# Kernel tuning notes

Measured on AMD Instinct MI355X. Metric: run time of the kernel, lower is better.

## Reference

```python
import jax, jax.numpy as jnp
import numpy as np

N_NODES = 100000
N_REL = 500
N_EDGES = 600000
DIM = 128


def setup_inputs() -> dict:
    key = jax.random.key(0)
    ks = jax.random.split(key, 10)
    ent = jax.random.normal(ks[0], (N_NODES, DIM), dtype=jnp.float32)
    rel = jax.random.normal(ks[1], (N_REL, DIM), dtype=jnp.float32)
    edge_index = jax.random.randint(ks[2], (2, N_EDGES), 0, N_NODES, dtype=jnp.int64)
    edge_type = jax.random.randint(ks[3], (N_EDGES,), 0, N_REL, dtype=jnp.int64)
    s = 1.0 / np.sqrt(DIM)
    W_self = jax.random.uniform(ks[4], (DIM, DIM), jnp.float32, -s, s)
    b_self = jax.random.uniform(ks[5], (DIM,), jnp.float32, -s, s)
    W_nei = jax.random.uniform(ks[6], (DIM, DIM), jnp.float32, -s, s)
    b_nei = jax.random.uniform(ks[7], (DIM,), jnp.float32, -s, s)
    W_rel = jax.random.uniform(ks[8], (DIM, DIM), jnp.float32, -s, s)
    b_rel = jax.random.uniform(ks[9], (DIM,), jnp.float32, -s, s)
    return {
        "ent": ent, "rel": rel, "edge_index": edge_index, "edge_type": edge_type,
        "W_self": W_self, "b_self": b_self,
        "W_nei": W_nei, "b_nei": b_nei,
        "W_rel": W_rel, "b_rel": b_rel,
    }


def reference(ent, rel, edge_index, edge_type, W_self, b_self, W_nei, b_nei, W_rel, b_rel):
    src, dst = edge_index[0], edge_index[1]
    # gather -> sigmoid-gate -> scatter-add
    msg = ent[src] * jax.nn.sigmoid(rel[edge_type])          # [E, dim]
    agg = jax.ops.segment_sum(msg, dst, num_segments=ent.shape[0])  # [N, dim]
    out_ent = jax.nn.relu(ent @ W_self.T + b_self + agg @ W_nei.T + b_nei)
    out_rel = rel @ W_rel.T + b_rel
    return (out_ent, out_rel)
```

## Files before the change

### kernel.cpp

```cpp
#include <hip/hip_runtime.h>
#include <hip/hip_bf16.h>
#include <math.h>

#define DIM 128

typedef __bf16 bf8 __attribute__((ext_vector_type(8)));
typedef float f4 __attribute__((ext_vector_type(4)));

struct __align__(8) bf16x4 { __hip_bfloat162 a, b; };

__global__ __launch_bounds__(256) void prep_kernel(
    const float* __restrict__ rel,
    const float* __restrict__ Ws,
    const float* __restrict__ Wn,
    const float* __restrict__ Wr,
    __hip_bfloat16* __restrict__ sigb,
    __hip_bfloat16* __restrict__ Wcat,
    float* __restrict__ Wt_rel,
    int* __restrict__ offs,
    int nSig, int sigBlocks, int N) {
    int b = blockIdx.x;
    if (b < sigBlocks) {
        int i = b * 256 + threadIdx.x;
        if (i < nSig) {
            float x = rel[i];
            sigb[i] = __float2bfloat16(1.0f / (1.0f + expf(-x)));
        }
    } else if (b < sigBlocks + 32) {
        int idx = (b - sigBlocks) * 256 + threadIdx.x;
        int j  = idx >> 6;
        int k0 = (idx & 63) * 4;
        const float* src = (k0 < DIM) ? &Ws[j * DIM + k0] : &Wn[j * DIM + (k0 - DIM)];
        float4 v = *(const float4*)src;
        bf16x4 o;
        o.a.x = __float2bfloat16(v.x);
        o.a.y = __float2bfloat16(v.y);
        o.b.x = __float2bfloat16(v.z);
        o.b.y = __float2bfloat16(v.w);
        *(bf16x4*)&Wcat[(size_t)j * 256 + k0] = o;
    } else if (b < sigBlocks + 32 + 64) {
        int id = (b - sigBlocks - 32) * 256 + threadIdx.x;
        int k = id >> 7;
        int j = id & 127;
        Wt_rel[id] = Wr[j * DIM + k];
    } else {
        int i = (b - sigBlocks - 32 - 64) * 256 + threadIdx.x;
        if (i <= N) offs[i] = 0;
    }
}

__global__ __launch_bounds__(256) void conv_hist_kernel(
    const float* __restrict__ ent,
    __hip_bfloat16* __restrict__ xcat,
    const int* __restrict__ edge_index,
    int* __restrict__ counts,
    int N, int E, int convBlocks) {
    if ((int)blockIdx.x < convBlocks) {
        long long tid = (long long)blockIdx.x * 256 + threadIdx.x;
        int row = (int)(tid >> 5);
        int q   = (int)(tid & 31);
        if (row >= N) return;
        float4 v = *(const float4*)&ent[(size_t)row * DIM + q * 4];
        bf16x4 o;
        o.a.x = __float2bfloat16(v.x);
        o.a.y = __float2bfloat16(v.y);
        o.b.x = __float2bfloat16(v.z);
        o.b.y = __float2bfloat16(v.w);
        *(bf16x4*)&xcat[(size_t)row * 256 + q * 4] = o;
    } else {
        int e = (blockIdx.x - convBlocks) * 256 + threadIdx.x;
        if (e < E) atomicAdd(&counts[edge_index[E + e]], 1);
    }
}

#define SCAN_TPB 256
#define SCAN_IPT 4
#define SCAN_IPB 1024

__global__ void scan_pass1(int* __restrict__ data,
                           int* __restrict__ blockSums, int N) {
    __shared__ int ts[SCAN_TPB];
    int t = threadIdx.x;
    int base = blockIdx.x * SCAN_IPB + t * SCAN_IPT;
    int v[SCAN_IPT];
    int s = 0;
    #pragma unroll
    for (int i = 0; i < SCAN_IPT; ++i) {
        int idx = base + i;
        v[i] = (idx < N) ? data[idx] : 0;
        s += v[i];
    }
    ts[t] = s;
    __syncthreads();
    for (int off = 1; off < SCAN_TPB; off <<= 1) {
        int x = (t >= off) ? ts[t - off] : 0;
        __syncthreads();
        ts[t] += x;
        __syncthreads();
    }
    int excl = ts[t] - s;
    #pragma unroll
    for (int i = 0; i < SCAN_IPT; ++i) {
        int idx = base + i;
        if (idx < N) data[idx] = excl;
        excl += v[i];
    }
    if (t == SCAN_TPB - 1) blockSums[blockIdx.x] = ts[t];
}

__global__ void scan_pass2(int* __restrict__ blockSums, int nb) {
    __shared__ int s[128];
    int t = threadIdx.x;
    int v = (t < nb) ? blockSums[t] : 0;
    s[t] = v;
    __syncthreads();
    for (int off = 1; off < 128; off <<= 1) {
        int x = (t >= off) ? s[t - off] : 0;
        __syncthreads();
        s[t] += x;
        __syncthreads();
    }
    if (t < nb) blockSums[t] = s[t] - v;
}

__global__ void scan_pass3(int* __restrict__ offs, const int* __restrict__ blockSums,
                           int* __restrict__ cursor, int N, int E) {
    int i = blockIdx.x * blockDim.x + threadIdx.x;
    if (i < N) {
        int o = offs[i] + blockSums[i >> 10];
        offs[i] = o;
        cursor[i] = o;
    }
    if (i == 0) offs[N] = E;
}

__global__ void scatter_ids_kernel(const int* __restrict__ edge_index,
                                   const int* __restrict__ edge_type,
                                   int* __restrict__ cursor,
                                   unsigned* __restrict__ spack, int E) {
    int e = blockIdx.x * blockDim.x + threadIdx.x;
    if (e >= E) return;
    int dst = edge_index[E + e];
    int p = atomicAdd(&cursor[dst], 1);
    spack[p] = (unsigned)edge_index[e] | ((unsigned)edge_type[e] << 17);
}

__global__ __launch_bounds__(256) void aggregate_kernel(
    const __hip_bfloat16* __restrict__ xcat,
    const __hip_bfloat16* __restrict__ sigb,
    const int* __restrict__ offs,
    const unsigned* __restrict__ spack,
    __hip_bfloat16* __restrict__ xcat_w, int N) {
    int wid  = (int)((blockIdx.x * (long long)blockDim.x + threadIdx.x) >> 6);
    int lane = threadIdx.x & 63;
    if (wid >= N) return;
    int beg = offs[wid], end = offs[wid + 1];
    float ax0 = 0.f, ay0 = 0.f, ax1 = 0.f, ay1 = 0.f;
    for (int e = beg; e < end; e += 4) {
        int r = end - e;
        unsigned p0 = spack[e];
        unsigned p1 = spack[r > 1 ? e + 1 : e];
        unsigned p2 = spack[r > 2 ? e + 2 : e];
        unsigned p3 = spack[r > 3 ? e + 3 : e];
        __hip_bfloat162 v0 = *(const __hip_bfloat162*)&xcat[(size_t)(p0 & 0x1FFFFu) * 256 + lane * 2];
        __hip_bfloat162 v1 = *(const __hip_bfloat162*)&xcat[(size_t)(p1 & 0x1FFFFu) * 256 + lane * 2];
        __hip_bfloat162 v2 = *(const __hip_bfloat162*)&xcat[(size_t)(p2 & 0x1FFFFu) * 256 + lane * 2];
        __hip_bfloat162 v3 = *(const __hip_bfloat162*)&xcat[(size_t)(p3 & 0x1FFFFu) * 256 + lane * 2];
        __hip_bfloat162 g0 = *(const __hip_bfloat162*)&sigb[(size_t)(p0 >> 17) * DIM + lane * 2];
        __hip_bfloat162 g1 = *(const __hip_bfloat162*)&sigb[(size_t)(p1 >> 17) * DIM + lane * 2];
        __hip_bfloat162 g2 = *(const __hip_bfloat162*)&sigb[(size_t)(p2 >> 17) * DIM + lane * 2];
        __hip_bfloat162 g3 = *(const __hip_bfloat162*)&sigb[(size_t)(p3 >> 17) * DIM + lane * 2];
        float m1 = (r > 1) ? 1.f : 0.f;
        float m2 = (r > 2) ? 1.f : 0.f;
        float m3 = (r > 3) ? 1.f : 0.f;
        ax0 += __bfloat162float(v0.x) * __bfloat162float(g0.x);
        ay0 += __bfloat162float(v0.y) * __bfloat162float(g0.y);
        ax1 += m1 * (__bfloat162float(v1.x) * __bfloat162float(g1.x));
        ay1 += m1 * (__bfloat162float(v1.y) * __bfloat162float(g1.y));
        ax0 += m2 * (__bfloat162float(v2.x) * __bfloat162float(g2.x));
        ay0 += m2 * (__bfloat162float(v2.y) * __bfloat162float(g2.y));
        ax1 += m3 * (__bfloat162float(v3.x) * __bfloat162float(g3.x));
        ay1 += m3 * (__bfloat162float(v3.y) * __bfloat162float(g3.y));
    }
    __hip_bfloat162 o;
    o.x = __float2bfloat16(ax0 + ax1);
    o.y = __float2bfloat16(ay0 + ay1);
    *(__hip_bfloat162*)&xcat_w[(size_t)wid * 256 + 128 + lane * 2] = o;
}

__global__ __launch_bounds__(128) void relout_kernel(
    const float* __restrict__ rel,
    const float* __restrict__ Wt_rel,
    const float* __restrict__ b_rel,
    float* __restrict__ out_rel) {
    __shared__ float rrow[DIM];
    int b = blockIdx.x;
    int t = threadIdx.x;
    rrow[t] = rel[(size_t)b * DIM + t];
    __syncthreads();
    float acc = b_rel[t];
    #pragma unroll 8
    for (int k = 0; k < DIM; ++k) {
        acc += rrow[k] * Wt_rel[k * DIM + t];
    }
    out_rel[(size_t)b * DIM + t] = acc;
}

__global__ __launch_bounds__(256) void gemm_mfma_kernel(
    const __hip_bfloat16* xcat,
    const __hip_bfloat16* __restrict__ Wcat,
    const float* __restrict__ b_self,
    const float* __restrict__ b_nei,
    float* out, int N) {
    __shared__ __hip_bfloat16 Bs[128][264];

    int t    = threadIdx.x;
    int wave = t >> 6;
    int lane = t & 63;
    int quad = lane >> 4;
    int r16  = lane & 15;

    {
        int r = t >> 1, h = t & 1;
        const float4* src = (const float4*)&Wcat[(size_t)r * 256 + h * 128];
        #pragma unroll
        for (int i = 0; i < 16; ++i) {
            *(float4*)&Bs[r][h * 128 + i * 8] = src[i];
        }
    }
    __syncthreads();

    int row0 = blockIdx.x * 128 + wave * 32;

    bf8 x[2][8];
    #pragma unroll
    for (int mt = 0; mt < 2; ++mt) {
        int m = row0 + mt * 16 + r16;
        if (m > N - 1) m = N - 1;
        const __hip_bfloat16* xp = &xcat[(size_t)m * 256 + quad * 8];
        #pragma unroll
        for (int ks = 0; ks < 8; ++ks) {
            x[mt][ks] = *(const bf8*)(xp + ks * 32);
        }
    }

    f4 acc[2][8];
    #pragma unroll
    for (int mt = 0; mt < 2; ++mt)
        #pragma unroll
        for (int jt = 0; jt < 8; ++jt)
            acc[mt][jt] = (f4){0.f, 0.f, 0.f, 0.f};

    #pragma unroll
    for (int ks = 0; ks < 8; ++ks) {
        #pragma unroll
        for (int jt = 0; jt < 8; ++jt) {
            bf8 w = *(const bf8*)&Bs[jt * 16 + r16][ks * 32 + quad * 8];
            acc[0][jt] = __builtin_amdgcn_mfma_f32_16x16x32_bf16(w, x[0][ks], acc[0][jt], 0, 0, 0);
            acc[1][jt] = __builtin_amdgcn_mfma_f32_16x16x32_bf16(w, x[1][ks], acc[1][jt], 0, 0, 0);
        }
    }

    f4 bias4[8];
    #pragma unroll
    for (int jt = 0; jt < 8; ++jt) {
        const float4 bs = *(const float4*)&b_self[jt * 16 + quad * 4];
        const float4 bn = *(const float4*)&b_nei[jt * 16 + quad * 4];
        bias4[jt] = (f4){bs.x + bn.x, bs.y + bn.y, bs.z + bn.z, bs.w + bn.w};
    }

    #pragma unroll
    for (int mt = 0; mt < 2; ++mt) {
        int m = row0 + mt * 16 + r16;
        if (m < N) {
            #pragma unroll
            for (int jt = 0; jt < 8; ++jt) {
                f4 v = acc[mt][jt] + bias4[jt];
                float4 o;
                o.x = fmaxf(v[0], 0.f);
                o.y = fmaxf(v[1], 0.f);
                o.z = fmaxf(v[2], 0.f);
                o.w = fmaxf(v[3], 0.f);
                *(float4*)&out[(size_t)m * DIM + jt * 16 + quad * 4] = o;
            }
        }
    }
}

extern "C" void kernel_launch(void* const* d_in, const int* in_sizes, int n_in,
                              void* d_out, int out_size, void* d_ws, size_t ws_size,
                              hipStream_t stream) {
    const float* ent        = (const float*)d_in[0];
    const float* rel        = (const float*)d_in[1];
    const int*   edge_index = (const int*)d_in[2];
    const int*   edge_type  = (const int*)d_in[3];
    const float* W_self     = (const float*)d_in[4];
    const float* b_self     = (const float*)d_in[5];
    const float* W_nei      = (const float*)d_in[6];
    const float* b_nei      = (const float*)d_in[7];
    const float* W_rel      = (const float*)d_in[8];
    const float* b_rel      = (const float*)d_in[9];

    const int N = in_sizes[0] / DIM;
    const int R = in_sizes[1] / DIM;
    const int E = in_sizes[3];

    float* out     = (float*)d_out;
    float* out_rel = out + (size_t)N * DIM;
    __hip_bfloat16* xcat = (__hip_bfloat16*)d_out;

    __hip_bfloat16* sigb = (__hip_bfloat16*)d_ws;
    float* Wt_rel  = (float*)(sigb + (size_t)R * DIM);
    __hip_bfloat16* Wcat = (__hip_bfloat16*)(Wt_rel + DIM * DIM);
    int*   offs    = (int*)(Wcat + 128 * 256);
    int*   cursor  = offs + (N + 8);
    int*   bsums   = cursor + (N + 8);
    unsigned* spack = (unsigned*)(bsums + 128);

    const int nSig = R * DIM;
    const int sigBlocks = (nSig + 255) / 256;
    const int zeroBlocks = (N + 1 + 255) / 256;
    const int scanBlocks = (N + SCAN_IPB - 1) / SCAN_IPB;

    prep_kernel<<<sigBlocks + 32 + 64 + zeroBlocks, 256, 0, stream>>>(
        rel, W_self, W_nei, W_rel, sigb, Wcat, Wt_rel, offs, nSig, sigBlocks, N);

    {
        int convBlocks = (int)(((long long)N * 32 + 255) / 256);
        int histBlocks = (E + 255) / 256;
        conv_hist_kernel<<<convBlocks + histBlocks, 256, 0, stream>>>(
            ent, xcat, edge_index, offs, N, E, convBlocks);
    }

    scan_pass1<<<scanBlocks, SCAN_TPB, 0, stream>>>(offs, bsums, N);
    scan_pass2<<<1, 128, 0, stream>>>(bsums, scanBlocks);
    scan_pass3<<<(N + 255) / 256, 256, 0, stream>>>(offs, bsums, cursor, N, E);

    scatter_ids_kernel<<<(E + 255) / 256, 256, 0, stream>>>(
        edge_index, edge_type, cursor, spack, E);

    {
        long long threads = (long long)N * 64;
        aggregate_kernel<<<(int)((threads + 255) / 256), 256, 0, stream>>>(
            xcat, sigb, offs, spack, xcat, N);
    }

    relout_kernel<<<R, DIM, 0, stream>>>(rel, Wt_rel, b_rel, out_rel);

    {
        int blocks = (N + 127) / 128;
        gemm_mfma_kernel<<<blocks, 256, 0, stream>>>(xcat, Wcat, b_self, b_nei, out, N);
    }
}
```

Measured before the change: 252.6 us.

## Record edge ranks in histogram, merge scan passes, fuse relout into aggregation

```diff
diff --git a/kernel.cpp b/kernel.cpp
--- a/kernel.cpp
+++ b/kernel.cpp
@@ -54,6 +54,7 @@
     __hip_bfloat16* __restrict__ xcat,
     const int* __restrict__ edge_index,
     int* __restrict__ counts,
+    int* __restrict__ rank,
     int N, int E, int convBlocks) {
     if ((int)blockIdx.x < convBlocks) {
         long long tid = (long long)blockIdx.x * 256 + threadIdx.x;
@@ -69,7 +70,9 @@
         *(bf16x4*)&xcat[(size_t)row * 256 + q * 4] = o;
     } else {
         int e = (blockIdx.x - convBlocks) * 256 + threadIdx.x;
-        if (e < E) atomicAdd(&counts[edge_index[E + e]], 1);
+        if (e < E) {
+            rank[e] = atomicAdd(&counts[edge_index[E + e]], 1);
+        }
     }
 }
 
@@ -108,102 +111,106 @@
     if (t == SCAN_TPB - 1) blockSums[blockIdx.x] = ts[t];
 }
 
-__global__ void scan_pass2(int* __restrict__ blockSums, int nb) {
-    __shared__ int s[128];
+__global__ __launch_bounds__(256) void scan_finish_kernel(
+    int* __restrict__ offs, const int* __restrict__ blockSums,
+    int nb, int N, int E) {
+    __shared__ int ps[128];
+    __shared__ int eps[128];
     int t = threadIdx.x;
-    int v = (t < nb) ? blockSums[t] : 0;
-    s[t] = v;
+    int v = 0;
+    if (t < 128) {
+        v = (t < nb) ? blockSums[t] : 0;
+        ps[t] = v;
+    }
     __syncthreads();
     for (int off = 1; off < 128; off <<= 1) {
-        int x = (t >= off) ? s[t - off] : 0;
-        __syncthreads();
-        s[t] += x;
-        __syncthreads();
-    }
-    if (t < nb) blockSums[t] = s[t] - v;
-}
-
-__global__ void scan_pass3(int* __restrict__ offs, const int* __restrict__ blockSums,
-                           int* __restrict__ cursor, int N, int E) {
-    int i = blockIdx.x * blockDim.x + threadIdx.x;
-    if (i < N) {
-        int o = offs[i] + blockSums[i >> 10];
-        offs[i] = o;
-        cursor[i] = o;
-    }
-    if (i == 0) offs[N] = E;
+        int x = (t >= off && t < 128) ? ps[t - off] : 0;
+        __syncthreads();
+        if (t < 128) ps[t] += x;
+        __syncthreads();
+    }
+    if (t < 128) eps[t] = ps[t] - v;
+    __syncthreads();
+    int i = blockIdx.x * 256 + t;
+    if (i < N)  offs[i] += eps[i >> 10];
+    if (i == N) offs[N] = E;
 }
 
 __global__ void scatter_ids_kernel(const int* __restrict__ edge_index,
                                    const int* __restrict__ edge_type,
-                                   int* __restrict__ cursor,
+                                   const int* __restrict__ offs,
+                                   const int* __restrict__ rank,
                                    unsigned* __restrict__ spack, int E) {
     int e = blockIdx.x * blockDim.x + threadIdx.x;
     if (e >= E) return;
     int dst = edge_index[E + e];
-    int p = atomicAdd(&cursor[dst], 1);
+    int p = offs[dst] + rank[e];
     spack[p] = (unsigned)edge_index[e] | ((unsigned)edge_type[e] << 17);
 }
 
-__global__ __launch_bounds__(256) void aggregate_kernel(
+__global__ __launch_bounds__(256) void agg_relout_kernel(
     const __hip_bfloat16* __restrict__ xcat,
     const __hip_bfloat16* __restrict__ sigb,
     const int* __restrict__ offs,
     const unsigned* __restrict__ spack,
-    __hip_bfloat16* __restrict__ xcat_w, int N) {
-    int wid  = (int)((blockIdx.x * (long long)blockDim.x + threadIdx.x) >> 6);
-    int lane = threadIdx.x & 63;
-    if (wid >= N) return;
-    int beg = offs[wid], end = offs[wid + 1];
-    float ax0 = 0.f, ay0 = 0.f, ax1 = 0.f, ay1 = 0.f;
-    for (int e = beg; e < end; e += 4) {
-        int r = end - e;
-        unsigned p0 = spack[e];
-        unsigned p1 = spack[r > 1 ? e + 1 : e];
-        unsigned p2 = spack[r > 2 ? e + 2 : e];
-        unsigned p3 = spack[r > 3 ? e + 3 : e];
-        __hip_bfloat162 v0 = *(const __hip_bfloat162*)&xcat[(size_t)(p0 & 0x1FFFFu) * 256 + lane * 2];
-        __hip_bfloat162 v1 = *(const __hip_bfloat162*)&xcat[(size_t)(p1 & 0x1FFFFu) * 256 + lane * 2];
-        __hip_bfloat162 v2 = *(const __hip_bfloat162*)&xcat[(size_t)(p2 & 0x1FFFFu) * 256 + lane * 2];
-        __hip_bfloat162 v3 = *(const __hip_bfloat162*)&xcat[(size_t)(p3 & 0x1FFFFu) * 256 + lane * 2];
-        __hip_bfloat162 g0 = *(const __hip_bfloat162*)&sigb[(size_t)(p0 >> 17) * DIM + lane * 2];
-        __hip_bfloat162 g1 = *(const __hip_bfloat162*)&sigb[(size_t)(p1 >> 17) * DIM + lane * 2];
-        __hip_bfloat162 g2 = *(const __hip_bfloat162*)&sigb[(size_t)(p2 >> 17) * DIM + lane * 2];
-        __hip_bfloat162 g3 = *(const __hip_bfloat162*)&sigb[(size_t)(p3 >> 17) * DIM + lane * 2];
-        float m1 = (r > 1) ? 1.f : 0.f;
-        float m2 = (r > 2) ? 1.f : 0.f;
-        float m3 = (r > 3) ? 1.f : 0.f;
-        ax0 += __bfloat162float(v0.x) * __bfloat162float(g0.x);
-        ay0 += __bfloat162float(v0.y) * __bfloat162float(g0.y);
-        ax1 += m1 * (__bfloat162float(v1.x) * __bfloat162float(g1.x));
-        ay1 += m1 * (__bfloat162float(v1.y) * __bfloat162float(g1.y));
-        ax0 += m2 * (__bfloat162float(v2.x) * __bfloat162float(g2.x));
-        ay0 += m2 * (__bfloat162float(v2.y) * __bfloat162float(g2.y));
-        ax1 += m3 * (__bfloat162float(v3.x) * __bfloat162float(g3.x));
-        ay1 += m3 * (__bfloat162float(v3.y) * __bfloat162float(g3.y));
-    }
-    __hip_bfloat162 o;
-    o.x = __float2bfloat16(ax0 + ax1);
-    o.y = __float2bfloat16(ay0 + ay1);
-    *(__hip_bfloat162*)&xcat_w[(size_t)wid * 256 + 128 + lane * 2] = o;
-}
-
-__global__ __launch_bounds__(128) void relout_kernel(
+    __hip_bfloat16* __restrict__ xcat_w,
     const float* __restrict__ rel,
     const float* __restrict__ Wt_rel,
     const float* __restrict__ b_rel,
-    float* __restrict__ out_rel) {
-    __shared__ float rrow[DIM];
-    int b = blockIdx.x;
-    int t = threadIdx.x;
-    rrow[t] = rel[(size_t)b * DIM + t];
-    __syncthreads();
-    float acc = b_rel[t];
-    #pragma unroll 8
-    for (int k = 0; k < DIM; ++k) {
-        acc += rrow[k] * Wt_rel[k * DIM + t];
-    }
-    out_rel[(size_t)b * DIM + t] = acc;
+    float* __restrict__ out_rel,
+    int N, int R, int aggBlocks) {
+    if ((int)blockIdx.x < aggBlocks) {
+        int wid  = (int)((blockIdx.x * (long long)256 + threadIdx.x) >> 6);
+        int lane = threadIdx.x & 63;
+        if (wid >= N) return;
+        int beg = offs[wid], end = offs[wid + 1];
+        float ax0 = 0.f, ay0 = 0.f, ax1 = 0.f, ay1 = 0.f;
+        for (int e = beg; e < end; e += 4) {
+            int r = end - e;
+            unsigned p0 = spack[e];
+            unsigned p1 = spack[r > 1 ? e + 1 : e];
+            unsigned p2 = spack[r > 2 ? e + 2 : e];
+            unsigned p3 = spack[r > 3 ? e + 3 : e];
+            __hip_bfloat162 v0 = *(const __hip_bfloat162*)&xcat[(size_t)(p0 & 0x1FFFFu) * 256 + lane * 2];
+            __hip_bfloat162 v1 = *(const __hip_bfloat162*)&xcat[(size_t)(p1 & 0x1FFFFu) * 256 + lane * 2];
+            __hip_bfloat162 v2 = *(const __hip_bfloat162*)&xcat[(size_t)(p2 & 0x1FFFFu) * 256 + lane * 2];
+            __hip_bfloat162 v3 = *(const __hip_bfloat162*)&xcat[(size_t)(p3 & 0x1FFFFu) * 256 + lane * 2];
+            __hip_bfloat162 g0 = *(const __hip_bfloat162*)&sigb[(size_t)(p0 >> 17) * DIM + lane * 2];
+            __hip_bfloat162 g1 = *(const __hip_bfloat162*)&sigb[(size_t)(p1 >> 17) * DIM + lane * 2];
+            __hip_bfloat162 g2 = *(const __hip_bfloat162*)&sigb[(size_t)(p2 >> 17) * DIM + lane * 2];
+            __hip_bfloat162 g3 = *(const __hip_bfloat162*)&sigb[(size_t)(p3 >> 17) * DIM + lane * 2];
+            float m1 = (r > 1) ? 1.f : 0.f;
+            float m2 = (r > 2) ? 1.f : 0.f;
+            float m3 = (r > 3) ? 1.f : 0.f;
+            ax0 += __bfloat162float(v0.x) * __bfloat162float(g0.x);
+            ay0 += __bfloat162float(v0.y) * __bfloat162float(g0.y);
+            ax1 += m1 * (__bfloat162float(v1.x) * __bfloat162float(g1.x));
+            ay1 += m1 * (__bfloat162float(v1.y) * __bfloat162float(g1.y));
+            ax0 += m2 * (__bfloat162float(v2.x) * __bfloat162float(g2.x));
+            ay0 += m2 * (__bfloat162float(v2.y) * __bfloat162float(g2.y));
+            ax1 += m3 * (__bfloat162float(v3.x) * __bfloat162float(g3.x));
+            ay1 += m3 * (__bfloat162float(v3.y) * __bfloat162float(g3.y));
+        }
+        __hip_bfloat162 o;
+        o.x = __float2bfloat16(ax0 + ax1);
+        o.y = __float2bfloat16(ay0 + ay1);
+        *(__hip_bfloat162*)&xcat_w[(size_t)wid * 256 + 128 + lane * 2] = o;
+    } else {
+        __shared__ float rr[2][DIM];
+        int idx  = blockIdx.x - aggBlocks;
+        int half = threadIdx.x >> 7;
+        int col  = threadIdx.x & 127;
+        int row  = idx * 2 + half;
+        if (row < R) rr[half][col] = rel[(size_t)row * DIM + col];
+        __syncthreads();
+        if (row >= R) return;
+        float acc = b_rel[col];
+        #pragma unroll 8
+        for (int k = 0; k < DIM; ++k) {
+            acc += rr[half][k] * Wt_rel[k * DIM + col];
+        }
+        out_rel[(size_t)row * DIM + col] = acc;
+    }
 }
 
 __global__ __launch_bounds__(256) void gemm_mfma_kernel(
@@ -313,9 +320,9 @@
     float* Wt_rel  = (float*)(sigb + (size_t)R * DIM);
     __hip_bfloat16* Wcat = (__hip_bfloat16*)(Wt_rel + DIM * DIM);
     int*   offs    = (int*)(Wcat + 128 * 256);
-    int*   cursor  = offs + (N + 8);
-    int*   bsums   = cursor + (N + 8);
-    unsigned* spack = (unsigned*)(bsums + 128);
+    int*   bsums   = offs + (N + 8);
+    int*   rank    = bsums + 128;
+    unsigned* spack = (unsigned*)(rank + E);
 
     const int nSig = R * DIM;
     const int sigBlocks = (nSig + 255) / 256;
@@ -329,23 +336,23 @@
         int convBlocks = (int)(((long long)N * 32 + 255) / 256);
         int histBlocks = (E + 255) / 256;
         conv_hist_kernel<<<convBlocks + histBlocks, 256, 0, stream>>>(
-            ent, xcat, edge_index, offs, N, E, convBlocks);
+            ent, xcat, edge_index, offs, rank, N, E, convBlocks);
     }
 
     scan_pass1<<<scanBlocks, SCAN_TPB, 0, stream>>>(offs, bsums, N);
-    scan_pass2<<<1, 128, 0, stream>>>(bsums, scanBlocks);
-    scan_pass3<<<(N + 255) / 256, 256, 0, stream>>>(offs, bsums, cursor, N, E);
+    scan_finish_kernel<<<(N + 1 + 255) / 256, 256, 0, stream>>>(
+        offs, bsums, scanBlocks, N, E);
 
     scatter_ids_kernel<<<(E + 255) / 256, 256, 0, stream>>>(
-        edge_index, edge_type, cursor, spack, E);
+        edge_index, edge_type, offs, rank, spack, E);
 
     {
-        long long threads = (long long)N * 64;
-        aggregate_kernel<<<(int)((threads + 255) / 256), 256, 0, stream>>>(
-            xcat, sigb, offs, spack, xcat, N);
-    }
-
-    relout_kernel<<<R, DIM, 0, stream>>>(rel, Wt_rel, b_rel, out_rel);
+        int aggBlocks = (int)(((long long)N * 64 + 255) / 256);
+        int relBlocks = (R + 1) / 2;
+        agg_relout_kernel<<<aggBlocks + relBlocks, 256, 0, stream>>>(
+            xcat, sigb, offs, spack, xcat, rel, Wt_rel, b_rel, out_rel,
+            N, R, aggBlocks);
+    }
 
     {
         int blocks = (N + 127) / 128;
```

Result: faster. 226.5 us (-10.3%).
